# Optimization experiments

Measured on AMD Instinct MI355X. Metric: run time of the kernel, lower is better.

## Reference

```python
import jax, jax.numpy as jnp
import numpy as np

N_UNITS = 1024
D_K = 64
B, S = 4, 2048
NEG = 1.0e9


def setup_inputs() -> dict:
    key = jax.random.key(0)
    ks = jax.random.split(key, 11)
    k = float(np.sqrt(1.0 / N_UNITS))
    u = lambda kk, shape: jax.random.uniform(kk, shape, jnp.float32, -k, k)
    Q = jax.random.normal(ks[0], (B, S, N_UNITS), jnp.float32)
    K = jax.random.normal(ks[1], (B, S, N_UNITS), jnp.float32)
    V = jax.random.normal(ks[2], (B, S, N_UNITS), jnp.float32)
    mask = jax.random.randint(ks[3], (B, S, S), 0, 2, jnp.int32)
    return {
        "Q": Q, "K": K, "V": V, "mask": mask,
        "Wq_w": u(ks[4], (D_K, N_UNITS)), "Wq_b": u(ks[5], (D_K,)),
        "Wk_w": u(ks[6], (D_K, N_UNITS)), "Wk_b": u(ks[7], (D_K,)),
        "Wv_w": u(ks[8], (D_K, N_UNITS)), "Wv_b": u(ks[9], (D_K,)),
    }


def reference(Q, K, V, mask, Wq_w, Wq_b, Wk_w, Wk_b, Wv_w, Wv_b):
    # Linear projections (torch Linear: x @ W.T + b)
    Q_ = jnp.einsum('bsu,du->bsd', Q, Wq_w) + Wq_b  # [B,S,D_K]
    K_ = jnp.einsum('bsu,du->bsd', K, Wk_w) + Wk_b
    V_ = jnp.einsum('bsu,du->bsd', V, Wv_w) + Wv_b
    scores = jnp.einsum('bid,bjd->bij', Q_, K_) / jnp.sqrt(jnp.float32(D_K))
    m = mask.astype(jnp.float32)
    # custom multiplicative-additive mask: scores*mask - 1e9*(1-mask)
    masked = scores * m - NEG * (1.0 - m)
    attn = jax.nn.softmax(masked, axis=-1)
    # dropout p=0.0 -> identity
    return jnp.einsum('bij,bjd->bid', attn, V_)
```

## Files before the change

### kernel.cpp

```cpp
#include <hip/hip_runtime.h>
#include <stdint.h>

#define S_ 2048
#define SS_ (S_ * S_)

typedef __bf16 bf16x8 __attribute__((ext_vector_type(8)));
typedef float f32x4 __attribute__((ext_vector_type(4)));
typedef unsigned int u32x4 __attribute__((ext_vector_type(4)));

union FragU {
    u32x4 u;
    bf16x8 v;
    unsigned short s[8];
};

__device__ __forceinline__ unsigned short f2bf(float f) {
    unsigned int u = __builtin_bit_cast(unsigned int, f);
    u += 0x7fffu + ((u >> 16) & 1u);
    return (unsigned short)(u >> 16);
}

__global__ __launch_bounds__(256) void cvt_w_kernel(
    const float* __restrict__ wq, const float* __restrict__ wk,
    const float* __restrict__ wv, unsigned short* __restrict__ out)
{
    int i = blockIdx.x * 256 + threadIdx.x;
    int mat = i >> 14;
    int off = (i & 16383) << 2;
    const float* src = (mat == 0) ? wq : (mat == 1) ? wk : wv;
    float4 v = *(const float4*)(src + off);
    ushort4 o;
    o.x = f2bf(v.x); o.y = f2bf(v.y); o.z = f2bf(v.z); o.w = f2bf(v.w);
    *(ushort4*)(out + mat * 65536 + off) = o;
}

__global__ __launch_bounds__(64) void proj_kernel(
    const float* __restrict__ Q, const float* __restrict__ K, const float* __restrict__ V,
    const unsigned short* __restrict__ Wb,
    const float* __restrict__ Bq, const float* __restrict__ Bk, const float* __restrict__ Bv,
    unsigned short* __restrict__ Qb, unsigned short* __restrict__ Kb,
    unsigned short* __restrict__ Vt)
{
    const int lane = threadIdx.x;
    const int lm = lane & 15, quad = lane >> 4;
    const int mat = blockIdx.y;
    const int row0 = blockIdx.x * 16;

    const float* X    = (mat == 0) ? Q  : (mat == 1) ? K  : V;
    const float* Bias = (mat == 0) ? Bq : (mat == 1) ? Bk : Bv;
    const unsigned short* W = Wb + mat * (64 * 1024);

    f32x4 acc[4];
    #pragma unroll
    for (int ct = 0; ct < 4; ++ct) { f32x4 z = {0.f,0.f,0.f,0.f}; acc[ct] = z; }

    const float* aptr = X + (row0 + lm) * 1024 + quad * 8;

    for (int k0 = 0; k0 < 1024; k0 += 32) {
        FragU af;
        float4 a0 = *(const float4*)(aptr + k0);
        float4 a1 = *(const float4*)(aptr + k0 + 4);
        af.s[0] = f2bf(a0.x); af.s[1] = f2bf(a0.y); af.s[2] = f2bf(a0.z); af.s[3] = f2bf(a0.w);
        af.s[4] = f2bf(a1.x); af.s[5] = f2bf(a1.y); af.s[6] = f2bf(a1.z); af.s[7] = f2bf(a1.w);
        #pragma unroll
        for (int ct = 0; ct < 4; ++ct) {
            FragU bfr;
            bfr.u = *(const u32x4*)(W + (ct * 16 + lm) * 1024 + k0 + quad * 8);
            acc[ct] = __builtin_amdgcn_mfma_f32_16x16x32_bf16(af.v, bfr.v, acc[ct], 0, 0, 0);
        }
    }

    #pragma unroll
    for (int ct = 0; ct < 4; ++ct) {
        int col = ct * 16 + lm;
        float bv = Bias[col];
        #pragma unroll
        for (int r = 0; r < 4; ++r) {
            int row = row0 + quad * 4 + r;
            unsigned short h = f2bf(acc[ct][r] + bv);
            if (mat == 0)      Qb[row * 64 + col] = h;
            else if (mat == 1) Kb[row * 64 + col] = h;
            else               Vt[(row >> 11) * (64 * 2048) + col * 2048 + (row & 2047)] = h;
        }
    }
}

__global__ __launch_bounds__(256) void attn_kernel(
    const unsigned short* __restrict__ Qb, const unsigned short* __restrict__ Kb,
    const unsigned short* __restrict__ Vt, const int* __restrict__ mask,
    float* __restrict__ out)
{
    const int tid = threadIdx.x;
    const int w = tid >> 6;
    const int lane = tid & 63;
    const int lm = lane & 15, quad = lane >> 4;
    const int b = blockIdx.y;
    const int q0 = blockIdx.x * 16;

    __shared__ unsigned short Plds[4][16 * 80];
    __shared__ float Olds[4][16 * 64];
    __shared__ float mlds[4][16];
    __shared__ float llds[4][16];

    FragU qf0, qf1;
    const unsigned short* qptr = Qb + (b * 2048 + q0 + lm) * 64 + quad * 8;
    qf0.u = *(const u32x4*)(qptr);
    qf1.u = *(const u32x4*)(qptr + 32);

    f32x4 o[4];
    #pragma unroll
    for (int dt = 0; dt < 4; ++dt) { f32x4 z = {0.f,0.f,0.f,0.f}; o[dt] = z; }
    float mrun[4] = {-3e38f, -3e38f, -3e38f, -3e38f};
    float lrun[4] = {0.f, 0.f, 0.f, 0.f};

    const int* mbase = mask + b * SS_;
    int rowoff[4];
    #pragma unroll
    for (int r = 0; r < 4; ++r) rowoff[r] = (q0 + quad * 4 + r) * S_;

    for (int iter = 0; iter < 8; ++iter) {
        const int k0 = w * 512 + iter * 64;

        f32x4 sc[4];
        #pragma unroll
        for (int ct = 0; ct < 4; ++ct) {
            f32x4 a = {0.f,0.f,0.f,0.f};
            const unsigned short* kptr = Kb + (b * 2048 + k0 + ct * 16 + lm) * 64 + quad * 8;
            FragU kf0, kf1;
            kf0.u = *(const u32x4*)(kptr);
            kf1.u = *(const u32x4*)(kptr + 32);
            a = __builtin_amdgcn_mfma_f32_16x16x32_bf16(qf0.v, kf0.v, a, 0, 0, 0);
            a = __builtin_amdgcn_mfma_f32_16x16x32_bf16(qf1.v, kf1.v, a, 0, 0, 0);
            sc[ct] = a;
        }

        #pragma unroll
        for (int ct = 0; ct < 4; ++ct) {
            #pragma unroll
            for (int r = 0; r < 4; ++r) {
                int key = k0 + ct * 16 + lm;
                int mv = mbase[rowoff[r] + key];
                float s = sc[ct][r] * 0.125f;
                sc[ct][r] = mv ? s : -1.0e9f;
            }
        }

        float alpha[4];
        #pragma unroll
        for (int r = 0; r < 4; ++r) {
            float vmx = fmaxf(fmaxf(sc[0][r], sc[1][r]), fmaxf(sc[2][r], sc[3][r]));
            #pragma unroll
            for (int off = 1; off <= 8; off <<= 1)
                vmx = fmaxf(vmx, __shfl_xor(vmx, off, 64));
            float mnew = fmaxf(mrun[r], vmx);
            alpha[r] = __expf(mrun[r] - mnew);
            mrun[r] = mnew;
            float rs = 0.f;
            #pragma unroll
            for (int ct = 0; ct < 4; ++ct) {
                float pv = __expf(sc[ct][r] - mnew);
                sc[ct][r] = pv;
                rs += pv;
            }
            #pragma unroll
            for (int off = 1; off <= 8; off <<= 1)
                rs += __shfl_xor(rs, off, 64);
            lrun[r] = lrun[r] * alpha[r] + rs;
        }

        #pragma unroll
        for (int dt = 0; dt < 4; ++dt)
            #pragma unroll
            for (int r = 0; r < 4; ++r)
                o[dt][r] *= alpha[r];

        #pragma unroll
        for (int ct = 0; ct < 4; ++ct)
            #pragma unroll
            for (int r = 0; r < 4; ++r)
                Plds[w][(quad * 4 + r) * 80 + ct * 16 + lm] = f2bf(sc[ct][r]);
        __syncthreads();

        #pragma unroll
        for (int ks = 0; ks < 2; ++ks) {
            FragU pf;
            pf.u = *(const u32x4*)&Plds[w][lm * 80 + ks * 32 + quad * 8];
            #pragma unroll
            for (int dt = 0; dt < 4; ++dt) {
                FragU vf;
                vf.u = *(const u32x4*)(Vt + b * (64 * 2048) + (dt * 16 + lm) * 2048
                                       + k0 + ks * 32 + quad * 8);
                o[dt] = __builtin_amdgcn_mfma_f32_16x16x32_bf16(pf.v, vf.v, o[dt], 0, 0, 0);
            }
        }
        __syncthreads();
    }

    #pragma unroll
    for (int dt = 0; dt < 4; ++dt)
        #pragma unroll
        for (int r = 0; r < 4; ++r)
            Olds[w][(quad * 4 + r) * 64 + dt * 16 + lm] = o[dt][r];
    if (lm == 0) {
        #pragma unroll
        for (int r = 0; r < 4; ++r) {
            mlds[w][quad * 4 + r] = mrun[r];
            llds[w][quad * 4 + r] = lrun[r];
        }
    }
    __syncthreads();

    #pragma unroll
    for (int i = 0; i < 4; ++i) {
        int e = i * 256 + tid;
        int q = e >> 6, d = e & 63;
        float m0 = mlds[0][q], m1 = mlds[1][q], m2 = mlds[2][q], m3 = mlds[3][q];
        float M = fmaxf(fmaxf(m0, m1), fmaxf(m2, m3));
        float e0 = __expf(m0 - M), e1 = __expf(m1 - M), e2 = __expf(m2 - M), e3 = __expf(m3 - M);
        float L = llds[0][q] * e0 + llds[1][q] * e1 + llds[2][q] * e2 + llds[3][q] * e3;
        float val = Olds[0][q * 64 + d] * e0 + Olds[1][q * 64 + d] * e1
                  + Olds[2][q * 64 + d] * e2 + Olds[3][q * 64 + d] * e3;
        out[(b * 2048 + q0 + q) * 64 + d] = val / L;
    }
}

extern "C" void kernel_launch(void* const* d_in, const int* in_sizes, int n_in,
                              void* d_out, int out_size, void* d_ws, size_t ws_size,
                              hipStream_t stream) {
    const float* Q   = (const float*)d_in[0];
    const float* K   = (const float*)d_in[1];
    const float* V   = (const float*)d_in[2];
    const int* mask  = (const int*)d_in[3];
    const float* Wq  = (const float*)d_in[4];
    const float* bq  = (const float*)d_in[5];
    const float* Wk  = (const float*)d_in[6];
    const float* bk  = (const float*)d_in[7];
    const float* Wv  = (const float*)d_in[8];
    const float* bv  = (const float*)d_in[9];
    float* out = (float*)d_out;

    char* ws = (char*)d_ws;
    unsigned short* Qb = (unsigned short*)(ws);
    unsigned short* Kb = (unsigned short*)(ws + (1u << 20));
    unsigned short* Vt = (unsigned short*)(ws + (2u << 20));
    unsigned short* Wb = (unsigned short*)(ws + (3u << 20));

    hipLaunchKernelGGL(cvt_w_kernel, dim3(192), dim3(256), 0, stream, Wq, Wk, Wv, Wb);
    hipLaunchKernelGGL(proj_kernel, dim3(512, 3), dim3(64), 0, stream,
                       Q, K, V, Wb, bq, bk, bv, Qb, Kb, Vt);
    hipLaunchKernelGGL(attn_kernel, dim3(128, 4), dim3(256), 0, stream,
                       Qb, Kb, Vt, mask, out);
}
```

Measured before the change: 228.8 us.

## Split-K projection across four waves and use eight key-split waves in attention

The projection kernel now uses 4 waves per block, each covering a quarter of the 1024-wide reduction, and combines the partial sums through shared memory before adding bias. The attention kernel doubles to 8 waves per block, each handling 256 keys, and the final merge of partial softmax states runs over 8 waves. The per-iteration block barriers are removed because each wave touches only its own P buffer. This raises parallelism and memory-level concurrency in both kernels, at the cost of more shared memory and a larger cross-wave merge.

Result: slower. 237.6 us (+3.9%).

```diff
diff --git a/kernel.cpp b/kernel.cpp
--- a/kernel.cpp
+++ b/kernel.cpp
@@ -34,18 +34,22 @@
     *(ushort4*)(out + mat * 65536 + off) = o;
 }
 
-__global__ __launch_bounds__(64) void proj_kernel(
+__global__ __launch_bounds__(256) void proj_kernel(
     const float* __restrict__ Q, const float* __restrict__ K, const float* __restrict__ V,
     const unsigned short* __restrict__ Wb,
     const float* __restrict__ Bq, const float* __restrict__ Bk, const float* __restrict__ Bv,
     unsigned short* __restrict__ Qb, unsigned short* __restrict__ Kb,
     unsigned short* __restrict__ Vt)
 {
-    const int lane = threadIdx.x;
+    const int tid = threadIdx.x;
+    const int w = tid >> 6;
+    const int lane = tid & 63;
     const int lm = lane & 15, quad = lane >> 4;
     const int mat = blockIdx.y;
     const int row0 = blockIdx.x * 16;
 
+    __shared__ float red[4][16 * 64];
+
     const float* X    = (mat == 0) ? Q  : (mat == 1) ? K  : V;
     const float* Bias = (mat == 0) ? Bq : (mat == 1) ? Bk : Bv;
     const unsigned short* W = Wb + mat * (64 * 1024);
@@ -54,9 +58,12 @@
     #pragma unroll
     for (int ct = 0; ct < 4; ++ct) { f32x4 z = {0.f,0.f,0.f,0.f}; acc[ct] = z; }
 
-    const float* aptr = X + (row0 + lm) * 1024 + quad * 8;
-
-    for (int k0 = 0; k0 < 1024; k0 += 32) {
+    const float* aptr = X + (row0 + lm) * 1024 + w * 256 + quad * 8;
+    const unsigned short* wbase = W + lm * 1024 + w * 256 + quad * 8;
+
+    #pragma unroll
+    for (int it = 0; it < 8; ++it) {
+        const int k0 = it * 32;
         FragU af;
         float4 a0 = *(const float4*)(aptr + k0);
         float4 a1 = *(const float4*)(aptr + k0 + 4);
@@ -65,27 +72,33 @@
         #pragma unroll
         for (int ct = 0; ct < 4; ++ct) {
             FragU bfr;
-            bfr.u = *(const u32x4*)(W + (ct * 16 + lm) * 1024 + k0 + quad * 8);
+            bfr.u = *(const u32x4*)(wbase + ct * 16 * 1024 + k0);
             acc[ct] = __builtin_amdgcn_mfma_f32_16x16x32_bf16(af.v, bfr.v, acc[ct], 0, 0, 0);
         }
     }
 
     #pragma unroll
-    for (int ct = 0; ct < 4; ++ct) {
-        int col = ct * 16 + lm;
-        float bv = Bias[col];
-        #pragma unroll
-        for (int r = 0; r < 4; ++r) {
-            int row = row0 + quad * 4 + r;
-            unsigned short h = f2bf(acc[ct][r] + bv);
-            if (mat == 0)      Qb[row * 64 + col] = h;
-            else if (mat == 1) Kb[row * 64 + col] = h;
-            else               Vt[(row >> 11) * (64 * 2048) + col * 2048 + (row & 2047)] = h;
-        }
-    }
-}
-
-__global__ __launch_bounds__(256) void attn_kernel(
+    for (int ct = 0; ct < 4; ++ct)
+        #pragma unroll
+        for (int r = 0; r < 4; ++r)
+            red[w][(quad * 4 + r) * 64 + ct * 16 + lm] = acc[ct][r];
+    __syncthreads();
+
+    #pragma unroll
+    for (int i = 0; i < 4; ++i) {
+        int e = i * 256 + tid;
+        int rl = e >> 6, col = e & 63;
+        float s = red[0][rl * 64 + col] + red[1][rl * 64 + col]
+                + red[2][rl * 64 + col] + red[3][rl * 64 + col] + Bias[col];
+        unsigned short h = f2bf(s);
+        int row = row0 + rl;
+        if (mat == 0)      Qb[row * 64 + col] = h;
+        else if (mat == 1) Kb[row * 64 + col] = h;
+        else               Vt[(row >> 11) * (64 * 2048) + col * 2048 + (row & 2047)] = h;
+    }
+}
+
+__global__ __launch_bounds__(512) void attn_kernel(
     const unsigned short* __restrict__ Qb, const unsigned short* __restrict__ Kb,
     const unsigned short* __restrict__ Vt, const int* __restrict__ mask,
     float* __restrict__ out)
@@ -97,10 +110,10 @@
     const int b = blockIdx.y;
     const int q0 = blockIdx.x * 16;
 
-    __shared__ unsigned short Plds[4][16 * 80];
-    __shared__ float Olds[4][16 * 64];
-    __shared__ float mlds[4][16];
-    __shared__ float llds[4][16];
+    __shared__ unsigned short Plds[8][16 * 80];
+    __shared__ float Olds[8][16 * 64];
+    __shared__ float mlds[8][16];
+    __shared__ float llds[8][16];
 
     FragU qf0, qf1;
     const unsigned short* qptr = Qb + (b * 2048 + q0 + lm) * 64 + quad * 8;
@@ -118,8 +131,9 @@
     #pragma unroll
     for (int r = 0; r < 4; ++r) rowoff[r] = (q0 + quad * 4 + r) * S_;
 
-    for (int iter = 0; iter < 8; ++iter) {
-        const int k0 = w * 512 + iter * 64;
+    #pragma unroll
+    for (int iter = 0; iter < 4; ++iter) {
+        const int k0 = w * 256 + iter * 64;
 
         f32x4 sc[4];
         #pragma unroll
@@ -179,7 +193,6 @@
             #pragma unroll
             for (int r = 0; r < 4; ++r)
                 Plds[w][(quad * 4 + r) * 80 + ct * 16 + lm] = f2bf(sc[ct][r]);
-        __syncthreads();
 
         #pragma unroll
         for (int ks = 0; ks < 2; ++ks) {
@@ -193,7 +206,6 @@
                 o[dt] = __builtin_amdgcn_mfma_f32_16x16x32_bf16(pf.v, vf.v, o[dt], 0, 0, 0);
             }
         }
-        __syncthreads();
     }
 
     #pragma unroll
@@ -211,15 +223,19 @@
     __syncthreads();
 
     #pragma unroll
-    for (int i = 0; i < 4; ++i) {
-        int e = i * 256 + tid;
+    for (int i = 0; i < 2; ++i) {
+        int e = i * 512 + tid;
         int q = e >> 6, d = e & 63;
-        float m0 = mlds[0][q], m1 = mlds[1][q], m2 = mlds[2][q], m3 = mlds[3][q];
-        float M = fmaxf(fmaxf(m0, m1), fmaxf(m2, m3));
-        float e0 = __expf(m0 - M), e1 = __expf(m1 - M), e2 = __expf(m2 - M), e3 = __expf(m3 - M);
-        float L = llds[0][q] * e0 + llds[1][q] * e1 + llds[2][q] * e2 + llds[3][q] * e3;
-        float val = Olds[0][q * 64 + d] * e0 + Olds[1][q * 64 + d] * e1
-                  + Olds[2][q * 64 + d] * e2 + Olds[3][q * 64 + d] * e3;
+        float M = -3e38f;
+        #pragma unroll
+        for (int ww = 0; ww < 8; ++ww) M = fmaxf(M, mlds[ww][q]);
+        float L = 0.f, val = 0.f;
+        #pragma unroll
+        for (int ww = 0; ww < 8; ++ww) {
+            float ew = __expf(mlds[ww][q] - M);
+            L   += llds[ww][q] * ew;
+            val += Olds[ww][q * 64 + d] * ew;
+        }
         out[(b * 2048 + q0 + q) * 64 + d] = val / L;
     }
 }
@@ -246,8 +262,8 @@
     unsigned short* Wb = (unsigned short*)(ws + (3u << 20));
 
     hipLaunchKernelGGL(cvt_w_kernel, dim3(192), dim3(256), 0, stream, Wq, Wk, Wv, Wb);
-    hipLaunchKernelGGL(proj_kernel, dim3(512, 3), dim3(64), 0, stream,
+    hipLaunchKernelGGL(proj_kernel, dim3(512, 3), dim3(256), 0, stream,
                        Q, K, V, Wb, bq, bk, bv, Qb, Kb, Vt);
-    hipLaunchKernelGGL(attn_kernel, dim3(128, 4), dim3(256), 0, stream,
+    hipLaunchKernelGGL(attn_kernel, dim3(128, 4), dim3(512), 0, stream,
                        Qb, Kb, Vt, mask, out);
 }
```
